# Optimization experiments

Measured on AMD Instinct MI355X. Metric: run time of the kernel, lower is better.

Reference implementation:

```python
import jax, jax.numpy as jnp
import numpy as np

N_HEADS = 8
ROPE_BASE = 10000.0


def _rope(x, pos):
    # x: (BN, T, H, D); pos: (T,)
    D = x.shape[-1]
    inv_freq = 1.0 / (ROPE_BASE ** (jnp.arange(0, D, 2, dtype=jnp.float32) / D))  # (D/2,)
    ang = pos[:, None].astype(jnp.float32) * inv_freq[None, :]                    # (T, D/2)
    cos = jnp.concatenate([jnp.cos(ang), jnp.cos(ang)], axis=-1)[None, :, None, :]  # (1,T,1,D)
    sin = jnp.concatenate([jnp.sin(ang), jnp.sin(ang)], axis=-1)[None, :, None, :]
    x1, x2 = x[..., : D // 2], x[..., D // 2 :]
    rot = jnp.concatenate([-x2, x1], axis=-1)
    return x * cos + rot * sin


def setup_inputs() -> dict:
    key = jax.random.key(0)
    ks = jax.random.split(key, 5)
    B, T, N, E = 2, 1024, 4, 256
    s = 1.0 / np.sqrt(E)
    return {
        "input_tensor": jax.random.normal(ks[0], (B, T, N, E), dtype=jnp.float32),
        "w_attn": jax.random.normal(ks[1], (E, 3 * E), dtype=jnp.float32) * s,
        "b_attn": jnp.zeros((3 * E,), dtype=jnp.float32),
        "w_proj": jax.random.normal(ks[2], (E, E), dtype=jnp.float32) * s,
        "b_proj": jnp.zeros((E,), dtype=jnp.float32),
    }


def reference(input_tensor, w_attn, b_attn, w_proj, b_proj):
    B, T, N, E = input_tensor.shape
    H = N_HEADS
    D = E // H
    # (B,T,N,E) -> (B*N, T, E)
    x = jnp.transpose(input_tensor, (0, 2, 1, 3)).reshape(B * N, T, E)
    qkv = x @ w_attn + b_attn  # (BN, T, 3E)
    q, k, v = jnp.split(qkv, 3, axis=-1)
    q = q.reshape(B * N, T, H, D)
    k = k.reshape(B * N, T, H, D)
    v = v.reshape(B * N, T, H, D)
    pos = jnp.arange(T)
    q = _rope(q, pos)
    k = _rope(k, pos)
    # causal SDPA
    scale = 1.0 / jnp.sqrt(jnp.asarray(D, dtype=q.dtype))
    scores = jnp.einsum("bthd,bshd->bhts", q, k) * scale  # (BN,H,T,T)
    causal = jnp.tril(jnp.ones((T, T), dtype=bool))
    scores = jnp.where(causal[None, None], scores, jnp.finfo(scores.dtype).min)
    probs = jax.nn.softmax(scores, axis=-1)
    out = jnp.einsum("bhts,bshd->bthd", probs, v).reshape(B * N, T, E)
    out = out @ w_proj + b_proj
    # (BN,T,E) -> (B,T,N,E)
    return jnp.transpose(out.reshape(B, N, T, E), (0, 2, 1, 3))
```

## Files before the change

kernel.cpp:

```cpp
#include <hip/hip_runtime.h>
#include <hip/hip_bf16.h>

#define T_ 1024
#define NB 4
#define E_ 256
#define H_ 8
#define D_ 32
#define E3 768

typedef __attribute__((ext_vector_type(8))) short v8s;
typedef __attribute__((ext_vector_type(4))) float v4f;

#define EXP2F(x) __builtin_amdgcn_exp2f(x)

__device__ __forceinline__ unsigned short f2bf(float x) {
    union { float f; unsigned int u; } v; v.f = x;
    unsigned int r = v.u + 0x7fffu + ((v.u >> 16) & 1u);
    return (unsigned short)(r >> 16);
}
__device__ __forceinline__ unsigned int cvtpk(float lo, float hi) {
    unsigned int r;
    asm("v_cvt_pk_bf16_f32 %0, %1, %2" : "=v"(r) : "v"(lo), "v"(hi));
    return r;
}

#define KMUL   0.2550343f
#define SHIFTL 11.5415603f


__global__ __launch_bounds__(256) void qkv_mfma_kernel(
    const float* __restrict__ x,
    const float* __restrict__ w_attn,
    const float* __restrict__ b_attn,
    unsigned short* __restrict__ Qb, unsigned short* __restrict__ Kb,
    unsigned short* __restrict__ VW)
{
    __shared__ unsigned short WTs[64][264];

    const int tid  = threadIdx.x;
    const int wsb  = tid >> 6;
    const int lane = tid & 63;
    const int g = lane >> 4, c = lane & 15;
    const int m0 = blockIdx.x * 64 + wsb * 16;
    const int n0 = blockIdx.y * 64;
    const int bn = m0 >> 10;
    const int b  = bn >> 2, nidx = bn & 3;
    const int t_base = m0 & 1023;

    {
        const int c4 = (tid & 15) * 4;
        const int kr = tid >> 4;
        #pragma unroll
        for (int p = 0; p < 16; ++p) {
            const int k = p * 16 + kr;
            float4 w4 = *(const float4*)(w_attn + (size_t)k * E3 + n0 + c4);
            WTs[c4 + 0][k] = f2bf(w4.x);
            WTs[c4 + 1][k] = f2bf(w4.y);
            WTs[c4 + 2][k] = f2bf(w4.z);
            WTs[c4 + 3][k] = f2bf(w4.w);
        }
    }
    __syncthreads();

    const float* xrow = x + ((size_t)(b * T_ + t_base + c) * NB + nidx) * E_;

    v4f acc[4];
    #pragma unroll
    for (int tt = 0; tt < 4; ++tt) acc[tt] = (v4f){0.f, 0.f, 0.f, 0.f};

    #pragma unroll
    for (int k0 = 0; k0 < 256; k0 += 32) {
        float4 f0 = *(const float4*)(xrow + k0 + 8 * g);
        float4 f1 = *(const float4*)(xrow + k0 + 8 * g + 4);
        union { v8s v; uint4 u; } af;
        af.u.x = cvtpk(f0.x, f0.y);
        af.u.y = cvtpk(f0.z, f0.w);
        af.u.z = cvtpk(f1.x, f1.y);
        af.u.w = cvtpk(f1.z, f1.w);
        #pragma unroll
        for (int tt = 0; tt < 4; ++tt) {
            v8s bfrag = *(const v8s*)(&WTs[tt * 16 + c][k0 + 8 * g]);
            acc[tt] = __builtin_amdgcn_mfma_f32_16x16x32_bf16(af.v, bfrag, acc[tt], 0, 0, 0);
        }
    }

    float bias[4];
    #pragma unroll
    for (int tt = 0; tt < 4; ++tt) bias[tt] = b_attn[n0 + tt * 16 + c];

    const int type = n0 >> 8;
    const int nl0  = n0 & 255;

    if (type <= 1) {
        unsigned short* Dst = (type == 0) ? Qb : Kb;
        float sn[4], cs[4];
        {
            const float invf = __expf(-(float)c * 0.5756462732485115f);
            #pragma unroll
            for (int r = 0; r < 4; ++r)
                sincosf((float)(t_base + 4 * g + r) * invf, &sn[r], &cs[r]);
        }
        #pragma unroll
        for (int tt = 0; tt < 4; ++tt) {
            const int n_l = nl0 + tt * 16;
            const int h = n_l >> 5, d = (n_l & 31) + c;
            const int bh = bn * 8 + h;
            const float sgn = (tt & 1) ? 1.f : -1.f;
            const int  ptt = tt ^ 1;
            #pragma unroll
            for (int r = 0; r < 4; ++r) {
                float v0 = acc[tt][r] + bias[tt];
                float v1 = acc[ptt][r] + bias[ptt];
                float o  = v0 * cs[r] + sgn * v1 * sn[r];
                int   t  = t_base + 4 * g + r;
                Dst[((size_t)bh * T_ + t) * D_ + d] = f2bf(o);
            }
        }
    } else {
        const int wv_ = t_base >> 5;
        const int tw  = (t_base & 31) + 4 * g;
        const int pos0 = ((tw >> 4) & 1) * 4 + ((tw >> 2) & 3) * 8;
        #pragma unroll
        for (int tt = 0; tt < 4; ++tt) {
            const int n_l = nl0 + tt * 16;
            const int h = n_l >> 5, d = (n_l & 31) + c;
            const int bh = bn * 8 + h;
            ushort4 pk;
            pk.x = f2bf(acc[tt][0] + bias[tt]);
            pk.y = f2bf(acc[tt][1] + bias[tt]);
            pk.z = f2bf(acc[tt][2] + bias[tt]);
            pk.w = f2bf(acc[tt][3] + bias[tt]);
            *(ushort4*)(VW + (((size_t)bh * 32 + wv_) * 32 + d) * 32 + pos0) = pk;
        }
    }
}

__global__ __launch_bounds__(256) void attn_kernel(
    const unsigned short* __restrict__ Qb,
    const unsigned short* __restrict__ Kb,
    const unsigned short* __restrict__ VW,
    unsigned short* __restrict__ Ob)
{
    const int tid  = threadIdx.x;
    const int wv   = tid >> 6;
    const int lane = tid & 63;
    const int g = lane >> 4, c = lane & 15;
    const int bx = blockIdx.x;
    const int bh = bx & 63;
    const int k  = bx >> 6;

    const int qts[2] = { k + 8 * wv, k + 56 - 8 * wv };
    const int lim1 = qts[1] >> 1;

    v8s qf[2];
    #pragma unroll
    for (int j = 0; j < 2; ++j)
        qf[j] = *(const v8s*)(Qb + ((size_t)bh * T_ + qts[j] * 16 + c) * D_ + 8 * g);

    v4f o0[2], o1[2];
    float ll[2];
    #pragma unroll
    for (int j = 0; j < 2; ++j) {
        o0[j] = (v4f){0.f, 0.f, 0.f, 0.f};
        o1[j] = (v4f){0.f, 0.f, 0.f, 0.f};
        ll[j] = 0.f;
    }

    const unsigned short* Ksrc = Kb + (size_t)bh * T_ * D_;
    const unsigned short* Vsrc = VW + (size_t)bh * 32 * 1024;

    const int koff = c * 32 + 8 * g;
    const int voff = c * 32 + 8 * g;

    v8s kA_n  = *(const v8s*)(Ksrc + koff);
    v8s kB_n  = *(const v8s*)(Ksrc + 512 + koff);
    v8s vf0_n = *(const v8s*)(Vsrc + voff);
    v8s vf1_n = *(const v8s*)(Vsrc + 512 + voff);

    for (int w = 0; w <= lim1; ++w) {
        v8s kfA = kA_n, kfB = kB_n;
        v8s vf0 = vf0_n, vf1 = vf1_n;
        if (w < lim1) {
            const unsigned short* kp = Ksrc + (size_t)(w + 1) * 1024;
            const unsigned short* vp = Vsrc + (size_t)(w + 1) * 1024;
            kA_n  = *(const v8s*)(kp + koff);
            kB_n  = *(const v8s*)(kp + 512 + koff);
            vf0_n = *(const v8s*)(vp + voff);
            vf1_n = *(const v8s*)(vp + 512 + voff);
        }

        const int s0 = w * 32;
        #pragma unroll
        for (int j = 0; j < 2; ++j) {
            const int qt  = qts[j];
            const int lim = qt >> 1;
            if (lim < w) continue;
            const int q = qt * 16 + c;

            v4f zero = {0.f, 0.f, 0.f, 0.f};
            v4f sA = __builtin_amdgcn_mfma_f32_16x16x32_bf16(kfA, qf[j], zero, 0, 0, 0);
            v4f sB = __builtin_amdgcn_mfma_f32_16x16x32_bf16(kfB, qf[j], zero, 0, 0, 0);

            const bool diag = (lim == w);
            float p[8];
            #pragma unroll
            for (int r = 0; r < 4; ++r) {
                float pa = EXP2F(fmaf(sA[r], KMUL, -SHIFTL));
                float pb = EXP2F(fmaf(sB[r], KMUL, -SHIFTL));
                if (diag) {
                    if (s0 + 4 * g + r > q)      pa = 0.f;
                    if (s0 + 16 + 4 * g + r > q) pb = 0.f;
                }
                p[r] = pa; p[4 + r] = pb;
                ll[j] += pa + pb;
            }
            union { v8s v; uint4 u; } pu;
            pu.u.x = cvtpk(p[0], p[1]);
            pu.u.y = cvtpk(p[2], p[3]);
            pu.u.z = cvtpk(p[4], p[5]);
            pu.u.w = cvtpk(p[6], p[7]);
            o0[j] = __builtin_amdgcn_mfma_f32_16x16x32_bf16(pu.v, vf0, o0[j], 0, 0, 0);
            o1[j] = __builtin_amdgcn_mfma_f32_16x16x32_bf16(pu.v, vf1, o1[j], 0, 0, 0);
        }
    }

    const int bn = bh >> 3, h = bh & 7;
    #pragma unroll
    for (int j = 0; j < 2; ++j) {
        float l_s = ll[j];
        l_s += __shfl_xor(l_s, 16, 64);
        l_s += __shfl_xor(l_s, 32, 64);
        float linv = 1.0f / l_s;
        float lr[4];
        #pragma unroll
        for (int r = 0; r < 4; ++r) lr[r] = __shfl(linv, 4 * g + r, 64);
        const int q0 = qts[j] * 16;
        #pragma unroll
        for (int r = 0; r < 4; ++r) {
            unsigned short* Orow = Ob + ((size_t)bn * T_ + q0 + 4 * g + r) * E_ + h * D_;
            Orow[c]      = f2bf(o0[j][r] * lr[r]);
            Orow[16 + c] = f2bf(o1[j][r] * lr[r]);
        }
    }
}

__global__ __launch_bounds__(256) void proj_mfma_kernel(
    const unsigned short* __restrict__ Ob,
    const float* __restrict__ w_proj,
    const float* __restrict__ b_proj,
    float* __restrict__ out)
{
    __shared__ unsigned short WPs[64][264];

    const int tid  = threadIdx.x;
    const int wsb  = tid >> 6;
    const int lane = tid & 63;
    const int g = lane >> 4, c = lane & 15;
    const int m0 = blockIdx.x * 64 + wsb * 16;
    const int n0 = blockIdx.y * 64;
    const int bn = m0 >> 10;
    const int b  = bn >> 2, nidx = bn & 3;
    const int t_base = m0 & 1023;

    {
        const int c4 = (tid & 15) * 4;
        const int kr = tid >> 4;
        #pragma unroll
        for (int p = 0; p < 16; ++p) {
            const int k = p * 16 + kr;
            float4 w4 = *(const float4*)(w_proj + (size_t)k * E_ + n0 + c4);
            WPs[c4 + 0][k] = f2bf(w4.x);
            WPs[c4 + 1][k] = f2bf(w4.y);
            WPs[c4 + 2][k] = f2bf(w4.z);
            WPs[c4 + 3][k] = f2bf(w4.w);
        }
    }
    __syncthreads();

    const unsigned short* arow = Ob + ((size_t)bn * T_ + t_base + c) * E_;

    v4f acc[4];
    #pragma unroll
    for (int tt = 0; tt < 4; ++tt) acc[tt] = (v4f){0.f, 0.f, 0.f, 0.f};

    #pragma unroll
    for (int s = 0; s < 8; ++s) {
        v8s afrag = *(const v8s*)(arow + s * 32 + 8 * g);
        #pragma unroll
        for (int tt = 0; tt < 4; ++tt) {
            v8s bfrag = *(const v8s*)(&WPs[tt * 16 + c][s * 32 + 8 * g]);
            acc[tt] = __builtin_amdgcn_mfma_f32_16x16x32_bf16(afrag, bfrag, acc[tt], 0, 0, 0);
        }
    }

    #pragma unroll
    for (int tt = 0; tt < 4; ++tt) {
        const int n = n0 + tt * 16 + c;
        const float bp = b_proj[n];
        #pragma unroll
        for (int r = 0; r < 4; ++r) {
            const int t = t_base + 4 * g + r;
            out[((size_t)(b * T_ + t) * NB + nidx) * E_ + n] = acc[tt][r] + bp;
        }
    }
}

extern "C" void kernel_launch(void* const* d_in, const int* in_sizes, int n_in,
                              void* d_out, int out_size, void* d_ws, size_t ws_size,
                              hipStream_t stream)
{
    const float* x      = (const float*)d_in[0];
    const float* w_attn = (const float*)d_in[1];
    const float* b_attn = (const float*)d_in[2];
    const float* w_proj = (const float*)d_in[3];
    const float* b_proj = (const float*)d_in[4];
    float* out = (float*)d_out;

    unsigned short* Qb  = (unsigned short*)d_ws;
    unsigned short* Kb  = Qb + 2097152;
    unsigned short* VW  = Kb + 2097152;
    unsigned short* Ob  = VW + 2097152;

    qkv_mfma_kernel<<<dim3(128, 12), 256, 0, stream>>>(x, w_attn, b_attn, Qb, Kb, VW);
    attn_kernel<<<512, 256, 0, stream>>>(Qb, Kb, VW, Ob);
    proj_mfma_kernel<<<dim3(128, 4), 256, 0, stream>>>(Ob, w_proj, b_proj, out);
}
```

Measured before the change: 110.1 us.

## Reuse converted x fragments across three output column groups in QKV GEMM

Each QKV block now computes three 64-column groups instead of one, loading and converting its x rows to bf16 once into registers and reusing them across all three groups. The grid shrinks from 12 to 4 column blocks. This cuts redundant global reads and conversions of x. In exchange it uses more registers (12 accumulators plus 8 A fragments), launches fewer blocks, and adds serialized weight-tile staging with extra barriers.

```diff
diff --git a/kernel.cpp b/kernel.cpp
--- a/kernel.cpp
+++ b/kernel.cpp
@@ -26,7 +26,6 @@
 
 #define KMUL   0.2550343f
 #define SHIFTL 11.5415603f
-
 
 __global__ __launch_bounds__(256) void qkv_mfma_kernel(
     const float* __restrict__ x,
@@ -41,15 +40,36 @@
     const int wsb  = tid >> 6;
     const int lane = tid & 63;
     const int g = lane >> 4, c = lane & 15;
-    const int m0 = blockIdx.x * 64 + wsb * 16;
-    const int n0 = blockIdx.y * 64;
+    const int row = blockIdx.x, cg0 = blockIdx.y * 3;
+    const int m0 = row * 64 + wsb * 16;
     const int bn = m0 >> 10;
     const int b  = bn >> 2, nidx = bn & 3;
     const int t_base = m0 & 1023;
 
-    {
-        const int c4 = (tid & 15) * 4;
-        const int kr = tid >> 4;
+    const float* xrow = x + ((size_t)(b * T_ + t_base + c) * NB + nidx) * E_;
+
+    union { v8s v; uint4 u; } af[8];
+    #pragma unroll
+    for (int s = 0; s < 8; ++s) {
+        float4 f0 = *(const float4*)(xrow + s * 32 + 8 * g);
+        float4 f1 = *(const float4*)(xrow + s * 32 + 8 * g + 4);
+        af[s].u.x = cvtpk(f0.x, f0.y);
+        af[s].u.y = cvtpk(f0.z, f0.w);
+        af[s].u.z = cvtpk(f1.x, f1.y);
+        af[s].u.w = cvtpk(f1.z, f1.w);
+    }
+
+    v4f acc[12];
+    #pragma unroll
+    for (int i = 0; i < 12; ++i) acc[i] = (v4f){0.f, 0.f, 0.f, 0.f};
+
+    const int c4 = (tid & 15) * 4;
+    const int kr = tid >> 4;
+
+    #pragma unroll
+    for (int cc = 0; cc < 3; ++cc) {
+        const int n0 = (cg0 + cc) * 64;
+        if (cc) __syncthreads();
         #pragma unroll
         for (int p = 0; p < 16; ++p) {
             const int k = p * 16 + kr;
@@ -59,78 +79,68 @@
             WTs[c4 + 2][k] = f2bf(w4.z);
             WTs[c4 + 3][k] = f2bf(w4.w);
         }
-    }
-    __syncthreads();
-
-    const float* xrow = x + ((size_t)(b * T_ + t_base + c) * NB + nidx) * E_;
-
-    v4f acc[4];
-    #pragma unroll
-    for (int tt = 0; tt < 4; ++tt) acc[tt] = (v4f){0.f, 0.f, 0.f, 0.f};
-
-    #pragma unroll
-    for (int k0 = 0; k0 < 256; k0 += 32) {
-        float4 f0 = *(const float4*)(xrow + k0 + 8 * g);
-        float4 f1 = *(const float4*)(xrow + k0 + 8 * g + 4);
-        union { v8s v; uint4 u; } af;
-        af.u.x = cvtpk(f0.x, f0.y);
-        af.u.y = cvtpk(f0.z, f0.w);
-        af.u.z = cvtpk(f1.x, f1.y);
-        af.u.w = cvtpk(f1.z, f1.w);
-        #pragma unroll
-        for (int tt = 0; tt < 4; ++tt) {
-            v8s bfrag = *(const v8s*)(&WTs[tt * 16 + c][k0 + 8 * g]);
-            acc[tt] = __builtin_amdgcn_mfma_f32_16x16x32_bf16(af.v, bfrag, acc[tt], 0, 0, 0);
-        }
-    }
-
-    float bias[4];
-    #pragma unroll
-    for (int tt = 0; tt < 4; ++tt) bias[tt] = b_attn[n0 + tt * 16 + c];
-
-    const int type = n0 >> 8;
-    const int nl0  = n0 & 255;
-
-    if (type <= 1) {
-        unsigned short* Dst = (type == 0) ? Qb : Kb;
-        float sn[4], cs[4];
-        {
-            const float invf = __expf(-(float)c * 0.5756462732485115f);
+        __syncthreads();
+        #pragma unroll
+        for (int s = 0; s < 8; ++s) {
             #pragma unroll
-            for (int r = 0; r < 4; ++r)
-                sincosf((float)(t_base + 4 * g + r) * invf, &sn[r], &cs[r]);
-        }
-        #pragma unroll
-        for (int tt = 0; tt < 4; ++tt) {
-            const int n_l = nl0 + tt * 16;
-            const int h = n_l >> 5, d = (n_l & 31) + c;
-            const int bh = bn * 8 + h;
-            const float sgn = (tt & 1) ? 1.f : -1.f;
-            const int  ptt = tt ^ 1;
+            for (int tt = 0; tt < 4; ++tt) {
+                v8s bfrag = *(const v8s*)(&WTs[tt * 16 + c][s * 32 + 8 * g]);
+                acc[cc * 4 + tt] = __builtin_amdgcn_mfma_f32_16x16x32_bf16(af[s].v, bfrag, acc[cc * 4 + tt], 0, 0, 0);
+            }
+        }
+    }
+
+    float sn[4], cs[4];
+    {
+        const float invf = __expf(-(float)c * 0.5756462732485115f);
+        #pragma unroll
+        for (int r = 0; r < 4; ++r)
+            sincosf((float)(t_base + 4 * g + r) * invf, &sn[r], &cs[r]);
+    }
+
+    #pragma unroll
+    for (int cc = 0; cc < 3; ++cc) {
+        const int n0 = (cg0 + cc) * 64;
+        const int type = n0 >> 8;
+        const int nl0  = n0 & 255;
+        float bias[4];
+        #pragma unroll
+        for (int tt = 0; tt < 4; ++tt) bias[tt] = b_attn[n0 + tt * 16 + c];
+
+        if (type <= 1) {
+            unsigned short* Dst = (type == 0) ? Qb : Kb;
             #pragma unroll
-            for (int r = 0; r < 4; ++r) {
-                float v0 = acc[tt][r] + bias[tt];
-                float v1 = acc[ptt][r] + bias[ptt];
-                float o  = v0 * cs[r] + sgn * v1 * sn[r];
-                int   t  = t_base + 4 * g + r;
-                Dst[((size_t)bh * T_ + t) * D_ + d] = f2bf(o);
+            for (int tt = 0; tt < 4; ++tt) {
+                const int n_l = nl0 + tt * 16;
+                const int h = n_l >> 5, d = (n_l & 31) + c;
+                const int bh = bn * 8 + h;
+                const float sgn = (tt & 1) ? 1.f : -1.f;
+                const int  ptt = tt ^ 1;
+                #pragma unroll
+                for (int r = 0; r < 4; ++r) {
+                    float v0 = acc[cc * 4 + tt][r] + bias[tt];
+                    float v1 = acc[cc * 4 + ptt][r] + bias[ptt];
+                    float o  = v0 * cs[r] + sgn * v1 * sn[r];
+                    int   t  = t_base + 4 * g + r;
+                    Dst[((size_t)bh * T_ + t) * D_ + d] = f2bf(o);
+                }
             }
-        }
-    } else {
-        const int wv_ = t_base >> 5;
-        const int tw  = (t_base & 31) + 4 * g;
-        const int pos0 = ((tw >> 4) & 1) * 4 + ((tw >> 2) & 3) * 8;
-        #pragma unroll
-        for (int tt = 0; tt < 4; ++tt) {
-            const int n_l = nl0 + tt * 16;
-            const int h = n_l >> 5, d = (n_l & 31) + c;
-            const int bh = bn * 8 + h;
-            ushort4 pk;
-            pk.x = f2bf(acc[tt][0] + bias[tt]);
-            pk.y = f2bf(acc[tt][1] + bias[tt]);
-            pk.z = f2bf(acc[tt][2] + bias[tt]);
-            pk.w = f2bf(acc[tt][3] + bias[tt]);
-            *(ushort4*)(VW + (((size_t)bh * 32 + wv_) * 32 + d) * 32 + pos0) = pk;
+        } else {
+            const int wv_ = t_base >> 5;
+            const int tw  = (t_base & 31) + 4 * g;
+            const int pos0 = ((tw >> 4) & 1) * 4 + ((tw >> 2) & 3) * 8;
+            #pragma unroll
+            for (int tt = 0; tt < 4; ++tt) {
+                const int n_l = nl0 + tt * 16;
+                const int h = n_l >> 5, d = (n_l & 31) + c;
+                const int bh = bn * 8 + h;
+                ushort4 pk;
+                pk.x = f2bf(acc[cc * 4 + tt][0] + bias[tt]);
+                pk.y = f2bf(acc[cc * 4 + tt][1] + bias[tt]);
+                pk.z = f2bf(acc[cc * 4 + tt][2] + bias[tt]);
+                pk.w = f2bf(acc[cc * 4 + tt][3] + bias[tt]);
+                *(ushort4*)(VW + (((size_t)bh * 32 + wv_) * 32 + d) * 32 + pos0) = pk;
+            }
         }
     }
 }
@@ -321,7 +331,7 @@
     unsigned short* VW  = Kb + 2097152;
     unsigned short* Ob  = VW + 2097152;
 
-    qkv_mfma_kernel<<<dim3(128, 12), 256, 0, stream>>>(x, w_attn, b_attn, Qb, Kb, VW);
+    qkv_mfma_kernel<<<dim3(128, 4), 256, 0, stream>>>(x, w_attn, b_attn, Qb, Kb, VW);
     attn_kernel<<<512, 256, 0, stream>>>(Qb, Kb, VW, Ob);
     proj_mfma_kernel<<<dim3(128, 4), 256, 0, stream>>>(Ob, w_proj, b_proj, out);
 }
```

Measured after the change: 116.3 us. 1.06x slower.
